# Performance work log

Hardware: AMD Instinct MI355X
Metric: run time of the kernel (lower is better)

## Reference

```python
import jax, jax.numpy as jnp
import numpy as np

HEAD_SIZE = 64
D_MODEL = 768


def setup_inputs() -> dict:
    key = jax.random.key(0)
    ks = jax.random.split(key, 7)
    x = jax.random.normal(ks[0], (8, 4096, D_MODEL), dtype=jnp.float32)
    def lin_init(kw, kb, fan_in, fan_out):
        bound = 1.0 / np.sqrt(fan_in)
        W = jax.random.uniform(kw, (fan_in, fan_out), minval=-bound, maxval=bound, dtype=jnp.float32)
        b = jax.random.uniform(kb, (fan_out,), minval=-bound, maxval=bound, dtype=jnp.float32)
        return W, b
    Wq, bq = lin_init(ks[1], ks[2], D_MODEL, HEAD_SIZE)
    Wk, bk = lin_init(ks[3], ks[4], D_MODEL, HEAD_SIZE)
    Wv, bv = lin_init(ks[5], ks[6], D_MODEL, HEAD_SIZE)
    return {"x": x, "Wq": Wq, "bq": bq, "Wk": Wk, "bk": bk, "Wv": Wv, "bv": bv}


def reference(x, Wq, bq, Wk, bk, Wv, bv):
    # x: [B, N, 768]; projections to [B, N, head_size]
    q = jnp.einsum("bnd,dh->bnh", x, Wq) + bq
    k = jnp.einsum("bnd,dh->bnh", x, Wk) + bk
    v = jnp.einsum("bnd,dh->bnh", x, Wv) + bv
    scale = 1.0 / jnp.sqrt(jnp.asarray(q.shape[-1], dtype=q.dtype))
    wei = jnp.einsum("bqh,bkh->bqk", q, k) * scale  # [B, N, N]
    wei = jax.nn.softmax(wei, axis=-1)
    out = jnp.einsum("bqk,bkh->bqh", wei, v)  # [B, N, head_size]
    return out
```

## Files before the change

kernel.cpp:

```cpp
#include <hip/hip_runtime.h>
#include <stdint.h>
#include <stddef.h>

typedef __bf16 bf16x8 __attribute__((ext_vector_type(8)));
typedef __bf16 bf16x4 __attribute__((ext_vector_type(4)));
typedef float  f32x4  __attribute__((ext_vector_type(4)));

#define MFMA16(A, B, C) __builtin_amdgcn_mfma_f32_16x16x32_bf16((A), (B), (C), 0, 0, 0)

#define QSCALE 0.18033688011112042f

#if __has_builtin(__builtin_amdgcn_exp2f)
__device__ __forceinline__ float fast_exp2(float x) {
    return __builtin_amdgcn_exp2f(x);
}
#else
__device__ __forceinline__ float fast_exp2(float x) {
    float r;
    asm("v_exp_f32 %0, %1" : "=v"(r) : "v"(x));
    return r;
}
#endif

__device__ __forceinline__ void async_copy16(__bf16* lds, const __bf16* g) {
    __builtin_amdgcn_global_load_lds(
        (const __attribute__((address_space(1))) void*)g,
        (__attribute__((address_space(3))) void*)lds,
        16, 0, 0);
}

__global__ __launch_bounds__(256) void qkv_proj_kernel(
    const float* __restrict__ x,
    const float* __restrict__ Wq, const float* __restrict__ bq,
    const float* __restrict__ Wk, const float* __restrict__ bk,
    const float* __restrict__ Wv, const float* __restrict__ bv,
    __bf16* __restrict__ Qg, __bf16* __restrict__ Kg, __bf16* __restrict__ Vpg)
{
    __shared__ __bf16 xs[64][40];
    __shared__ __bf16 wt[192][40];

    const int tid  = threadIdx.x;
    const int wid  = tid >> 6;
    const int lane = tid & 63;
    const int l15  = lane & 15;
    const int l4   = lane >> 4;
    const int m0   = blockIdx.x * 64;

    f32x4 acc[4][3];
    #pragma unroll
    for (int i = 0; i < 4; ++i)
        #pragma unroll
        for (int j = 0; j < 3; ++j)
            acc[i][j] = (f32x4){0.f, 0.f, 0.f, 0.f};

    for (int k0 = 0; k0 < 768; k0 += 32) {
        #pragma unroll
        for (int i = 0; i < 2; ++i) {
            int idx = tid + 256 * i;
            int row = idx >> 3;
            int c4  = idx & 7;
            const float4 v = *reinterpret_cast<const float4*>(
                x + (size_t)(m0 + row) * 768 + k0 + c4 * 4);
            bf16x4 t;
            t[0] = (__bf16)v.x; t[1] = (__bf16)v.y;
            t[2] = (__bf16)v.z; t[3] = (__bf16)v.w;
            *reinterpret_cast<bf16x4*>(&xs[row][c4 * 4]) = t;
        }
        #pragma unroll
        for (int i = 0; i < 6; ++i) {
            int idx = tid + 256 * i;
            int kg  = idx / 192;
            int c   = idx - kg * 192;
            const float* Wm = (c < 64) ? Wq : ((c < 128) ? Wk : Wv);
            int cc = c & 63;
            bf16x4 t;
            #pragma unroll
            for (int j = 0; j < 4; ++j)
                t[j] = (__bf16)Wm[(size_t)(k0 + kg * 4 + j) * 64 + cc];
            *reinterpret_cast<bf16x4*>(&wt[c][kg * 4]) = t;
        }
        __syncthreads();

        bf16x8 afrag[4];
        #pragma unroll
        for (int rf = 0; rf < 4; ++rf)
            afrag[rf] = *reinterpret_cast<const bf16x8*>(&xs[rf * 16 + l15][l4 * 8]);
        #pragma unroll
        for (int cf = 0; cf < 3; ++cf) {
            bf16x8 bfrag = *reinterpret_cast<const bf16x8*>(
                &wt[wid * 48 + cf * 16 + l15][l4 * 8]);
            #pragma unroll
            for (int rf = 0; rf < 4; ++rf)
                acc[rf][cf] = MFMA16(afrag[rf], bfrag, acc[rf][cf]);
        }
        __syncthreads();
    }

    #pragma unroll
    for (int cf = 0; cf < 3; ++cf) {
        int col = wid * 48 + cf * 16 + l15;
        int mi  = col >> 6;
        int h   = col & 63;
        float bias = (mi == 0) ? bq[h] : ((mi == 1) ? bk[h] : bv[h]);
        float scl  = (mi == 0) ? QSCALE : 1.0f;
        #pragma unroll
        for (int rf = 0; rf < 4; ++rf) {
            int r0 = rf * 16 + l4 * 4;
            if (mi == 2) {
                int m  = m0 + r0;
                int bb = m >> 12;
                int n0 = m & 4095;
                int n0p = (n0 & ~31) | (l4 * 8 + (rf & 1) * 4);
                bf16x4 t;
                #pragma unroll
                for (int r = 0; r < 4; ++r)
                    t[r] = (__bf16)(acc[rf][cf][r] + bias);
                *reinterpret_cast<bf16x4*>(
                    Vpg + ((size_t)bb * 64 + h) * 4096 + n0p) = t;
            } else {
                __bf16* G = (mi == 0) ? Qg : Kg;
                #pragma unroll
                for (int r = 0; r < 4; ++r)
                    G[(size_t)(m0 + r0 + r) * 64 + h] =
                        (__bf16)((acc[rf][cf][r] + bias) * scl);
            }
        }
    }
}

__global__ __launch_bounds__(512, 2) void attn_kernel(
    const __bf16* __restrict__ Qg, const __bf16* __restrict__ Kg,
    const __bf16* __restrict__ Vpg, float* __restrict__ out)
{
    __shared__ __align__(16) char smem[131072];
    __bf16* ksbase = reinterpret_cast<__bf16*>(smem);
    __bf16* vsbase = ksbase + 8 * 2 * 32 * 64;

    const int tid  = threadIdx.x;
    const int wid  = tid >> 6;
    const int lane = tid & 63;
    const int l15  = lane & 15;
    const int l4   = lane >> 4;
    const int ks   = wid;
    const int b    = blockIdx.x & 7;
    const int qt   = blockIdx.x >> 3;
    const int q0   = qt * 64;

    const __bf16* Kb = Kg  + (size_t)b * 4096 * 64;
    const __bf16* Vb = Vpg + (size_t)b * 64 * 4096;

    __bf16* kst0 = ksbase + (ks * 2 + 0) * 32 * 64;
    __bf16* kst1 = ksbase + (ks * 2 + 1) * 32 * 64;
    __bf16* vst0 = vsbase + (ks * 2 + 0) * 64 * 32;
    __bf16* vst1 = vsbase + (ks * 2 + 1) * 64 * 32;

    int koff[2][2], voff[4];
    #pragma unroll
    for (int dc = 0; dc < 2; ++dc)
        #pragma unroll
        for (int cf = 0; cf < 2; ++cf) {
            int row = cf * 16 + l15;
            koff[dc][cf] = row * 64 + (((dc * 4 + l4) ^ (row & 7)) * 8);
        }
    #pragma unroll
    for (int ht = 0; ht < 4; ++ht) {
        int row = ht * 16 + l15;
        voff[ht] = row * 32 + ((l4 ^ (row & 3)) * 8);
    }

    const int krow = lane >> 3;
    const int kg_s = (lane & 7) ^ (lane >> 3);
    const int vrow = lane >> 2;
    const int vg_s = (lane & 3) ^ ((lane >> 2) & 3);

    auto issue_stage = [&](__bf16* kp, __bf16* vp, int c) {
        #pragma unroll
        for (int j = 0; j < 4; ++j) {
            async_copy16(kp + j * 8 * 64,
                         Kb + (size_t)(c * 32 + j * 8 + krow) * 64 + kg_s * 8);
            async_copy16(vp + j * 16 * 32,
                         Vb + (size_t)(j * 16 + vrow) * 4096 + c * 32 + vg_s * 8);
        }
    };

    bf16x8 aq[4][2];
    #pragma unroll
    for (int set = 0; set < 4; ++set)
        #pragma unroll
        for (int dc = 0; dc < 2; ++dc)
            aq[set][dc] = *reinterpret_cast<const bf16x8*>(
                Qg + (size_t)(b * 4096 + q0 + set * 16 + l15) * 64 + dc * 32 + l4 * 8);

    f32x4 lacc[4];
    f32x4 o[4][4];
    #pragma unroll
    for (int set = 0; set < 4; ++set) {
        lacc[set] = (f32x4){0.f, 0.f, 0.f, 0.f};
        #pragma unroll
        for (int ht = 0; ht < 4; ++ht)
            o[set][ht] = (f32x4){0.f, 0.f, 0.f, 0.f};
    }

    const int c0 = ks * 16;
    issue_stage(kst0, vst0, c0);

    for (int t = 0; t < 16; ++t) {
        __syncthreads();
        const __bf16* kp = (t & 1) ? kst1 : kst0;
        const __bf16* vp = (t & 1) ? vst1 : vst0;
        __bf16* kpn = (t & 1) ? kst0 : kst1;
        __bf16* vpn = (t & 1) ? vst0 : vst1;
        const bool pre = (t + 1) < 16;
        if (pre) issue_stage(kpn, vpn, c0 + t + 1);

        f32x4 s[4][2];
        #pragma unroll
        for (int set = 0; set < 4; ++set)
            #pragma unroll
            for (int cf = 0; cf < 2; ++cf)
                s[set][cf] = (f32x4){0.f, 0.f, 0.f, 0.f};
        __builtin_amdgcn_s_setprio(1);
        #pragma unroll
        for (int dc = 0; dc < 2; ++dc)
            #pragma unroll
            for (int cf = 0; cf < 2; ++cf) {
                bf16x8 kf = *reinterpret_cast<const bf16x8*>(kp + koff[dc][cf]);
                #pragma unroll
                for (int set = 0; set < 4; ++set)
                    s[set][cf] = MFMA16(kf, aq[set][dc], s[set][cf]);
            }
        __builtin_amdgcn_s_setprio(0);

        #pragma unroll
        for (int set = 0; set < 4; ++set) {
            #pragma unroll
            for (int cf = 0; cf < 2; ++cf)
                #pragma unroll
                for (int r = 0; r < 4; ++r)
                    s[set][cf][r] = fast_exp2(s[set][cf][r]);
            lacc[set] += s[set][0];
            lacc[set] += s[set][1];
        }

        bf16x8 pb[4];
        #pragma unroll
        for (int set = 0; set < 4; ++set)
            #pragma unroll
            for (int j = 0; j < 4; ++j) {
                pb[set][j]     = (__bf16)s[set][0][j];
                pb[set][j + 4] = (__bf16)s[set][1][j];
            }

        __builtin_amdgcn_s_setprio(1);
        #pragma unroll
        for (int ht = 0; ht < 4; ++ht) {
            bf16x8 vf = *reinterpret_cast<const bf16x8*>(vp + voff[ht]);
            #pragma unroll
            for (int set = 0; set < 4; ++set)
                o[set][ht] = MFMA16(vf, pb[set], o[set][ht]);
        }
        __builtin_amdgcn_s_setprio(0);
    }

    float lw[4];
    #pragma unroll
    for (int set = 0; set < 4; ++set) {
        float v = lacc[set][0] + lacc[set][1] + lacc[set][2] + lacc[set][3];
        v += __shfl_xor(v, 16);
        v += __shfl_xor(v, 32);
        lw[set] = v;
    }

    __syncthreads();
    float* lbuf = reinterpret_cast<float*>(smem);
    float* obuf = lbuf + 512;
    const int hcol = 4 * l4;

    if (l4 == 0) {
        #pragma unroll
        for (int set = 0; set < 4; ++set)
            lbuf[ks * 64 + set * 16 + l15] = lw[set];
    }

    auto writeO = [&](int bufi) {
        #pragma unroll
        for (int set = 0; set < 4; ++set)
            #pragma unroll
            for (int ht = 0; ht < 4; ++ht)
                *reinterpret_cast<f32x4*>(
                    &obuf[bufi * 4352 + (set * 16 + l15) * 68 + ht * 16 + hcol]) =
                    o[set][ht];
    };
    auto addO = [&](int bufi) {
        #pragma unroll
        for (int set = 0; set < 4; ++set)
            #pragma unroll
            for (int ht = 0; ht < 4; ++ht) {
                f32x4 p = *reinterpret_cast<const f32x4*>(
                    &obuf[bufi * 4352 + (set * 16 + l15) * 68 + ht * 16 + hcol]);
                o[set][ht][0] += p[0]; o[set][ht][1] += p[1];
                o[set][ht][2] += p[2]; o[set][ht][3] += p[3];
            }
    };

    if (ks >= 4) writeO(ks - 4);
    __syncthreads();
    if (ks < 4) addO(ks);
    __syncthreads();
    if (ks == 2 || ks == 3) writeO(ks - 2);
    __syncthreads();
    if (ks < 2) addO(ks);
    __syncthreads();
    if (ks == 1) writeO(0);
    __syncthreads();
    if (ks == 0) {
        addO(0);
        #pragma unroll
        for (int set = 0; set < 4; ++set) {
            int q = set * 16 + l15;
            float L = 0.f;
            #pragma unroll
            for (int k = 0; k < 8; ++k)
                L += lbuf[k * 64 + q];
            float inv = 1.0f / L;
            #pragma unroll
            for (int ht = 0; ht < 4; ++ht) {
                f32x4 acc = o[set][ht];
                acc[0] *= inv; acc[1] *= inv; acc[2] *= inv; acc[3] *= inv;
                *reinterpret_cast<f32x4*>(
                    out + (size_t)(b * 4096 + q0 + q) * 64 + ht * 16 + hcol) = acc;
            }
        }
    }
}

extern "C" void kernel_launch(void* const* d_in, const int* in_sizes, int n_in,
                              void* d_out, int out_size, void* d_ws, size_t ws_size,
                              hipStream_t stream)
{
    (void)in_sizes; (void)n_in; (void)out_size; (void)ws_size;
    const float* x  = (const float*)d_in[0];
    const float* Wq = (const float*)d_in[1];
    const float* bq = (const float*)d_in[2];
    const float* Wk = (const float*)d_in[3];
    const float* bk = (const float*)d_in[4];
    const float* Wv = (const float*)d_in[5];
    const float* bv = (const float*)d_in[6];
    float* out = (float*)d_out;

    __bf16* Qg  = (__bf16*)d_ws;
    __bf16* Kg  = Qg + (size_t)32768 * 64;
    __bf16* Vpg = Kg + (size_t)32768 * 64;

    qkv_proj_kernel<<<512, 256, 0, stream>>>(x, Wq, bq, Wk, bk, Wv, bv, Qg, Kg, Vpg);
    attn_kernel<<<512, 512, 0, stream>>>(Qg, Kg, Vpg, out);
}
```

Baseline: 83.10 us.

## Halve attention block to 4 waves, drop per-tile barrier for per-wave waitcnt

The attention kernel now runs 4 waves per block instead of 8. Each wave covers 32 key chunks instead of 16, and LDS drops to 64KB. Because each wave owns its staging buffers, the per-iteration __syncthreads is replaced by an s_waitcnt vmcnt(0). K and V fragments are read from LDS into registers before the next prefetch is issued, and the cross-wave O reduction becomes a simpler serial accumulation over 4 waves. This removes block-wide barrier stalls and lets more blocks fit per CU, at the cost of a longer serial loop per wave and fewer waves per block to hide latency.

```diff
diff --git a/kernel.cpp b/kernel.cpp
--- a/kernel.cpp
+++ b/kernel.cpp
@@ -128,13 +128,13 @@
     }
 }
 
-__global__ __launch_bounds__(512, 2) void attn_kernel(
+__global__ __launch_bounds__(256, 2) void attn_kernel(
     const __bf16* __restrict__ Qg, const __bf16* __restrict__ Kg,
     const __bf16* __restrict__ Vpg, float* __restrict__ out)
 {
-    __shared__ __align__(16) char smem[131072];
+    __shared__ __align__(16) char smem[65536];
     __bf16* ksbase = reinterpret_cast<__bf16*>(smem);
-    __bf16* vsbase = ksbase + 8 * 2 * 32 * 64;
+    __bf16* vsbase = ksbase + 4 * 2 * 32 * 64;
 
     const int tid  = threadIdx.x;
     const int wid  = tid >> 6;
@@ -201,16 +201,29 @@
             o[set][ht] = (f32x4){0.f, 0.f, 0.f, 0.f};
     }
 
-    const int c0 = ks * 16;
+    const int c0 = ks * 32;
     issue_stage(kst0, vst0, c0);
 
-    for (int t = 0; t < 16; ++t) {
-        __syncthreads();
+    for (int t = 0; t < 32; ++t) {
+        asm volatile("s_waitcnt vmcnt(0)" ::: "memory");
+        __builtin_amdgcn_sched_barrier(0);
+
         const __bf16* kp = (t & 1) ? kst1 : kst0;
         const __bf16* vp = (t & 1) ? vst1 : vst0;
         __bf16* kpn = (t & 1) ? kst0 : kst1;
         __bf16* vpn = (t & 1) ? vst0 : vst1;
-        const bool pre = (t + 1) < 16;
+        const bool pre = (t + 1) < 32;
+
+        bf16x8 kfr[2][2], vfr[4];
+        #pragma unroll
+        for (int dc = 0; dc < 2; ++dc)
+            #pragma unroll
+            for (int cf = 0; cf < 2; ++cf)
+                kfr[dc][cf] = *reinterpret_cast<const bf16x8*>(kp + koff[dc][cf]);
+        #pragma unroll
+        for (int ht = 0; ht < 4; ++ht)
+            vfr[ht] = *reinterpret_cast<const bf16x8*>(vp + voff[ht]);
+
         if (pre) issue_stage(kpn, vpn, c0 + t + 1);
 
         f32x4 s[4][2];
@@ -223,12 +236,10 @@
         #pragma unroll
         for (int dc = 0; dc < 2; ++dc)
             #pragma unroll
-            for (int cf = 0; cf < 2; ++cf) {
-                bf16x8 kf = *reinterpret_cast<const bf16x8*>(kp + koff[dc][cf]);
+            for (int cf = 0; cf < 2; ++cf)
                 #pragma unroll
                 for (int set = 0; set < 4; ++set)
-                    s[set][cf] = MFMA16(kf, aq[set][dc], s[set][cf]);
-            }
+                    s[set][cf] = MFMA16(kfr[dc][cf], aq[set][dc], s[set][cf]);
         __builtin_amdgcn_s_setprio(0);
 
         #pragma unroll
@@ -253,12 +264,10 @@
 
         __builtin_amdgcn_s_setprio(1);
         #pragma unroll
-        for (int ht = 0; ht < 4; ++ht) {
-            bf16x8 vf = *reinterpret_cast<const bf16x8*>(vp + voff[ht]);
+        for (int ht = 0; ht < 4; ++ht)
             #pragma unroll
             for (int set = 0; set < 4; ++set)
-                o[set][ht] = MFMA16(vf, pb[set], o[set][ht]);
-        }
+                o[set][ht] = MFMA16(vfr[ht], pb[set], o[set][ht]);
         __builtin_amdgcn_s_setprio(0);
     }
 
@@ -273,7 +282,7 @@
 
     __syncthreads();
     float* lbuf = reinterpret_cast<float*>(smem);
-    float* obuf = lbuf + 512;
+    float* obuf = lbuf + 256;
     const int hcol = 4 * l4;
 
     if (l4 == 0) {
@@ -281,47 +290,36 @@
         for (int set = 0; set < 4; ++set)
             lbuf[ks * 64 + set * 16 + l15] = lw[set];
     }
-
-    auto writeO = [&](int bufi) {
-        #pragma unroll
-        for (int set = 0; set < 4; ++set)
-            #pragma unroll
-            for (int ht = 0; ht < 4; ++ht)
-                *reinterpret_cast<f32x4*>(
-                    &obuf[bufi * 4352 + (set * 16 + l15) * 68 + ht * 16 + hcol]) =
-                    o[set][ht];
-    };
-    auto addO = [&](int bufi) {
-        #pragma unroll
-        for (int set = 0; set < 4; ++set)
-            #pragma unroll
-            for (int ht = 0; ht < 4; ++ht) {
-                f32x4 p = *reinterpret_cast<const f32x4*>(
-                    &obuf[bufi * 4352 + (set * 16 + l15) * 68 + ht * 16 + hcol]);
-                o[set][ht][0] += p[0]; o[set][ht][1] += p[1];
-                o[set][ht][2] += p[2]; o[set][ht][3] += p[3];
-            }
-    };
-
-    if (ks >= 4) writeO(ks - 4);
-    __syncthreads();
-    if (ks < 4) addO(ks);
-    __syncthreads();
-    if (ks == 2 || ks == 3) writeO(ks - 2);
-    __syncthreads();
-    if (ks < 2) addO(ks);
-    __syncthreads();
-    if (ks == 1) writeO(0);
-    __syncthreads();
+    #pragma unroll
+    for (int k = 1; k < 4; ++k) {
+        if (ks == k) {
+            #pragma unroll
+            for (int set = 0; set < 4; ++set)
+                #pragma unroll
+                for (int ht = 0; ht < 4; ++ht)
+                    *reinterpret_cast<f32x4*>(
+                        &obuf[(set * 16 + l15) * 68 + ht * 16 + hcol]) = o[set][ht];
+        }
+        __syncthreads();
+        if (ks == 0) {
+            #pragma unroll
+            for (int set = 0; set < 4; ++set)
+                #pragma unroll
+                for (int ht = 0; ht < 4; ++ht) {
+                    f32x4 p = *reinterpret_cast<const f32x4*>(
+                        &obuf[(set * 16 + l15) * 68 + ht * 16 + hcol]);
+                    o[set][ht][0] += p[0]; o[set][ht][1] += p[1];
+                    o[set][ht][2] += p[2]; o[set][ht][3] += p[3];
+                }
+        }
+        __syncthreads();
+    }
+
     if (ks == 0) {
-        addO(0);
         #pragma unroll
         for (int set = 0; set < 4; ++set) {
             int q = set * 16 + l15;
-            float L = 0.f;
-            #pragma unroll
-            for (int k = 0; k < 8; ++k)
-                L += lbuf[k * 64 + q];
+            float L = lbuf[q] + lbuf[64 + q] + lbuf[128 + q] + lbuf[192 + q];
             float inv = 1.0f / L;
             #pragma unroll
             for (int ht = 0; ht < 4; ++ht) {
@@ -353,5 +351,5 @@
     __bf16* Vpg = Kg + (size_t)32768 * 64;
 
     qkv_proj_kernel<<<512, 256, 0, stream>>>(x, Wq, bq, Wk, bk, Wv, bv, Qg, Kg, Vpg);
-    attn_kernel<<<512, 512, 0, stream>>>(Qg, Kg, Vpg, out);
-}
+    attn_kernel<<<512, 256, 0, stream>>>(Qg, Kg, Vpg, out);
+}
```

After: 73.76 us. 1.13x faster.
